# Kernel tuning notes

Measured on AMD Instinct MI355X. Metric: run time of the kernel, lower is better.

The kernel has to match this reference:

```python
import jax, jax.numpy as jnp
import numpy as np

SEQ_DIM = 256
PAIR_DIM = 128
N_HEADS = 8
HIDDEN = 32
B, L = 4, 512


def layer_norm(x, gamma, beta, eps=1e-5):
    mu = jnp.mean(x, axis=-1, keepdims=True)
    var = jnp.var(x, axis=-1, keepdims=True)
    return (x - mu) * jax.lax.rsqrt(var + eps) * gamma + beta


def setup_inputs() -> dict:
    key = jax.random.key(0)
    ks = jax.random.split(key, 12)
    d = N_HEADS * HIDDEN
    s = 0.02
    return {
        "seq": jax.random.normal(ks[0], (B, L, SEQ_DIM), jnp.float32),
        "pair": jax.random.normal(ks[1], (B, L, L, PAIR_DIM), jnp.float32),
        "ln_seq_g": jnp.ones((SEQ_DIM,), jnp.float32),
        "ln_seq_b": jnp.zeros((SEQ_DIM,), jnp.float32),
        "ln_pair_g": jnp.ones((PAIR_DIM,), jnp.float32),
        "ln_pair_b": jnp.zeros((PAIR_DIM,), jnp.float32),
        "W_b": jax.random.normal(ks[2], (PAIR_DIM, N_HEADS), jnp.float32) * s,
        "W_q": jax.random.normal(ks[3], (SEQ_DIM, d), jnp.float32) * s,
        "W_k": jax.random.normal(ks[4], (SEQ_DIM, d), jnp.float32) * s,
        "W_v": jax.random.normal(ks[5], (SEQ_DIM, d), jnp.float32) * s,
        "W_g": jax.random.normal(ks[6], (SEQ_DIM, d), jnp.float32) * s,
        "b_g": jnp.zeros((d,), jnp.float32),
        "W_o": jax.random.normal(ks[7], (d, SEQ_DIM), jnp.float32) * s,
        "b_o": jnp.zeros((SEQ_DIM,), jnp.float32),
    }


def reference(seq, pair, ln_seq_g, ln_seq_b, ln_pair_g, ln_pair_b,
              W_b, W_q, W_k, W_v, W_g, b_g, W_o, b_o):
    b, l, _ = seq.shape
    factor = 1.0 / np.sqrt(HIDDEN).astype(np.float32)
    s = layer_norm(seq, ln_seq_g, ln_seq_b)
    p = layer_norm(pair, ln_pair_g, ln_pair_b)
    Q = (s @ W_q).reshape(b, l, N_HEADS, HIDDEN)
    K = (s @ W_k).reshape(b, l, N_HEADS, HIDDEN)
    V = (s @ W_v).reshape(b, l, N_HEADS, HIDDEN)
    # pair bias: [b, i, j, n] -> [b, n, i, j]
    bias = jnp.einsum('bijp,pn->bnij', p, W_b)
    att = jnp.einsum('binh,bjnh->bnij', Q, K) * factor + bias
    att = jax.nn.softmax(att, axis=-1)
    gate = jax.nn.sigmoid(s @ W_g + b_g).reshape(b, l, N_HEADS, HIDDEN)
    out = jnp.einsum('bnij,bjnh->binh', att, V) * gate
    out = out.reshape(b, l, N_HEADS * HIDDEN)
    return out @ W_o + b_o
```

## Files before the change

kernel.cpp:

```cpp
#include <hip/hip_runtime.h>
#include <math.h>

#define OFF_Q    0
#define OFF_K    (524288)
#define OFF_V    (524288*2)
#define OFF_G    (524288*3)
#define OFF_PRE  (524288*4)
#define OFF_BIAS (524288*5)

template <int CTRL>
__device__ __forceinline__ float dpp_mov(float x) {
  return __int_as_float(__builtin_amdgcn_update_dpp(0, __float_as_int(x), CTRL, 0xF, 0xF, true));
}
template <int CTRL>
__device__ __forceinline__ float dpp_add(float x) { return x + dpp_mov<CTRL>(x); }
__device__ __forceinline__ float red16(float v) {
  v = dpp_add<0xB1>(v);
  v = dpp_add<0x4E>(v);
  v = dpp_add<0x141>(v);
  v = dpp_add<0x140>(v);
  return v;
}

#define SEL8(a, f, out) do { \
  float _s0 = ((f)&1) ? a[1] : a[0]; \
  float _s1 = ((f)&1) ? a[3] : a[2]; \
  float _s2 = ((f)&1) ? a[5] : a[4]; \
  float _s3 = ((f)&1) ? a[7] : a[6]; \
  float _t0 = ((f)&2) ? _s1 : _s0; \
  float _t1 = ((f)&2) ? _s3 : _s2; \
  out = ((f)&4) ? _t1 : _t0; \
} while(0)

__device__ __forceinline__ float4 sel8_f4(const float4* a, int f) {
  float4 s0 = (f&1) ? a[1] : a[0];
  float4 s1 = (f&1) ? a[3] : a[2];
  float4 s2 = (f&1) ? a[5] : a[4];
  float4 s3 = (f&1) ? a[7] : a[6];
  float4 t0 = (f&2) ? s1 : s0;
  float4 t1 = (f&2) ? s3 : s2;
  return (f&4) ? t1 : t0;
}

__device__ __forceinline__ float dot4(float4 a, float4 b, float acc) {
  acc = fmaf(a.x, b.x, acc); acc = fmaf(a.y, b.y, acc);
  acc = fmaf(a.z, b.z, acc); return fmaf(a.w, b.w, acc);
}

template <int CTRL>
__device__ __forceinline__ void merge_dpp(float& m, float& l, float4* acc) {
  float m2 = dpp_mov<CTRL>(m);
  float l2 = dpp_mov<CTRL>(l);
  float M = fmaxf(m, m2);
  float ea = __expf(m - M), eb = __expf(m2 - M);
  l = l*ea + l2*eb;
#pragma unroll
  for (int x = 0; x < 8; ++x) {
    acc[x].x = acc[x].x*ea + dpp_mov<CTRL>(acc[x].x)*eb;
    acc[x].y = acc[x].y*ea + dpp_mov<CTRL>(acc[x].y)*eb;
    acc[x].z = acc[x].z*ea + dpp_mov<CTRL>(acc[x].z)*eb;
    acc[x].w = acc[x].w*ea + dpp_mov<CTRL>(acc[x].w)*eb;
  }
  m = M;
}

__global__ __launch_bounds__(256, 3) void k_mega(
    const float* __restrict__ seq, const float* __restrict__ lsg, const float* __restrict__ lsb,
    const float* __restrict__ lpg, const float* __restrict__ lpb, const float* __restrict__ Wb,
    const float* __restrict__ Wq, const float* __restrict__ Wk, const float* __restrict__ Wv,
    const float* __restrict__ Wg, const float* __restrict__ bg, const float* __restrict__ pair,
    float* __restrict__ Qw, float* __restrict__ Kw, float* __restrict__ Vw, float* __restrict__ Gw,
    float* __restrict__ biasw) {
  __shared__ __align__(16) float As[256*36];
  int t = threadIdx.x;
  int blk = blockIdx.x;

  if (blk >= 512) {
    int kb = blk - 512;
    int m0 = (kb >> 3) * 32;
    int y = kb & 7;
    {
      int r = t >> 3, c0 = t & 7;
      const float* srow = seq + (size_t)(m0 + r) * 256;
      float4 v[8];
      float s = 0.f, sq = 0.f;
#pragma unroll
      for (int qq = 0; qq < 8; ++qq) {
        v[qq] = *(const float4*)(srow + 4*(c0 + 8*qq));
        s += v[qq].x + v[qq].y + v[qq].z + v[qq].w;
        sq = fmaf(v[qq].x, v[qq].x, sq); sq = fmaf(v[qq].y, v[qq].y, sq);
        sq = fmaf(v[qq].z, v[qq].z, sq); sq = fmaf(v[qq].w, v[qq].w, sq);
      }
#pragma unroll
      for (int mm = 1; mm < 8; mm <<= 1) { s += __shfl_xor(s, mm); sq += __shfl_xor(sq, mm); }
      float mu = s * (1.f/256.f);
      float var = sq * (1.f/256.f) - mu*mu;
      float rstd = rsqrtf(var + 1e-5f);
#pragma unroll
      for (int qq = 0; qq < 8; ++qq) {
        int c4 = c0 + 8*qq;
        float4 g  = *(const float4*)(lsg + 4*c4);
        float4 bb = *(const float4*)(lsb + 4*c4);
        float* dp = As + 4*c4*36 + r;
        dp[0]   = (v[qq].x - mu)*rstd*g.x + bb.x;
        dp[36]  = (v[qq].y - mu)*rstd*g.y + bb.y;
        dp[72]  = (v[qq].z - mu)*rstd*g.z + bb.z;
        dp[108] = (v[qq].w - mu)*rstd*g.w + bb.w;
      }
    }
    __syncthreads();
    const float* Wm = (y < 2) ? Wq : (y < 4) ? Wk : (y < 6) ? Wv : Wg;
    int cb = (y & 1) * 128;
    int rg = t >> 5, cg2 = t & 31;
    const float* bp = Wm + cb + 4*cg2;
    const float* ap = As + 4*rg;
    float4 a0 = {0,0,0,0}, a1 = {0,0,0,0}, a2 = {0,0,0,0}, a3 = {0,0,0,0};
#pragma unroll 4
    for (int p = 0; p < 256; ++p) {
      float4 a  = *(const float4*)(ap + p*36);
      float4 bv = *(const float4*)(bp + p*256);
      a0.x = fmaf(a.x, bv.x, a0.x); a0.y = fmaf(a.x, bv.y, a0.y);
      a0.z = fmaf(a.x, bv.z, a0.z); a0.w = fmaf(a.x, bv.w, a0.w);
      a1.x = fmaf(a.y, bv.x, a1.x); a1.y = fmaf(a.y, bv.y, a1.y);
      a1.z = fmaf(a.y, bv.z, a1.z); a1.w = fmaf(a.y, bv.w, a1.w);
      a2.x = fmaf(a.z, bv.x, a2.x); a2.y = fmaf(a.z, bv.y, a2.y);
      a2.z = fmaf(a.z, bv.z, a2.z); a2.w = fmaf(a.z, bv.w, a2.w);
      a3.x = fmaf(a.w, bv.x, a3.x); a3.y = fmaf(a.w, bv.y, a3.y);
      a3.z = fmaf(a.w, bv.z, a3.z); a3.w = fmaf(a.w, bv.w, a3.w);
    }
    int mat = y >> 1;
    int col = cb + 4*cg2;
    float* outp = (mat == 0) ? Qw : (mat == 1) ? Kw : (mat == 2) ? Vw : Gw;
    if (mat == 0) {
      const float qs = 0.17677669529663687f;
      a0.x*=qs; a0.y*=qs; a0.z*=qs; a0.w*=qs;
      a1.x*=qs; a1.y*=qs; a1.z*=qs; a1.w*=qs;
      a2.x*=qs; a2.y*=qs; a2.z*=qs; a2.w*=qs;
      a3.x*=qs; a3.y*=qs; a3.z*=qs; a3.w*=qs;
    }
    if (mat == 3) {
      float4 g4 = *(const float4*)(bg + col);
      a0.x = 1.f/(1.f+__expf(-(a0.x+g4.x))); a0.y = 1.f/(1.f+__expf(-(a0.y+g4.y)));
      a0.z = 1.f/(1.f+__expf(-(a0.z+g4.z))); a0.w = 1.f/(1.f+__expf(-(a0.w+g4.w)));
      a1.x = 1.f/(1.f+__expf(-(a1.x+g4.x))); a1.y = 1.f/(1.f+__expf(-(a1.y+g4.y)));
      a1.z = 1.f/(1.f+__expf(-(a1.z+g4.z))); a1.w = 1.f/(1.f+__expf(-(a1.w+g4.w)));
      a2.x = 1.f/(1.f+__expf(-(a2.x+g4.x))); a2.y = 1.f/(1.f+__expf(-(a2.y+g4.y)));
      a2.z = 1.f/(1.f+__expf(-(a2.z+g4.z))); a2.w = 1.f/(1.f+__expf(-(a2.w+g4.w)));
      a3.x = 1.f/(1.f+__expf(-(a3.x+g4.x))); a3.y = 1.f/(1.f+__expf(-(a3.y+g4.y)));
      a3.z = 1.f/(1.f+__expf(-(a3.z+g4.z))); a3.w = 1.f/(1.f+__expf(-(a3.w+g4.w)));
    }
    int orow = m0 + 4*rg;
    *(float4*)(outp + (size_t)(orow+0)*256 + col) = a0;
    *(float4*)(outp + (size_t)(orow+1)*256 + col) = a1;
    *(float4*)(outp + (size_t)(orow+2)*256 + col) = a2;
    *(float4*)(outp + (size_t)(orow+3)*256 + col) = a3;
    return;
  }

  int lane = t & 63, w = t >> 6;
  int grp = lane >> 4, f = lane & 15;

  float wp[64];
  float cg[8] = {0,0,0,0,0,0,0,0}, cbv[8] = {0,0,0,0,0,0,0,0};
#pragma unroll
  for (int q = 0; q < 4; ++q) {
    int kA = 4*f + q, kB = 64 + 4*f + q;
    float gA = lpg[kA], bA = lpb[kA];
    float gB = lpg[kB], bB = lpb[kB];
    float4 uA0 = *(const float4*)(Wb + kA*8);
    float4 uA1 = *(const float4*)(Wb + kA*8 + 4);
    float4 uB0 = *(const float4*)(Wb + kB*8);
    float4 uB1 = *(const float4*)(Wb + kB*8 + 4);
    wp[q*8+0] = gA*uA0.x; cg[0] += wp[q*8+0]; cbv[0] = fmaf(bA, uA0.x, cbv[0]);
    wp[q*8+1] = gA*uA0.y; cg[1] += wp[q*8+1]; cbv[1] = fmaf(bA, uA0.y, cbv[1]);
    wp[q*8+2] = gA*uA0.z; cg[2] += wp[q*8+2]; cbv[2] = fmaf(bA, uA0.z, cbv[2]);
    wp[q*8+3] = gA*uA0.w; cg[3] += wp[q*8+3]; cbv[3] = fmaf(bA, uA0.w, cbv[3]);
    wp[q*8+4] = gA*uA1.x; cg[4] += wp[q*8+4]; cbv[4] = fmaf(bA, uA1.x, cbv[4]);
    wp[q*8+5] = gA*uA1.y; cg[5] += wp[q*8+5]; cbv[5] = fmaf(bA, uA1.y, cbv[5]);
    wp[q*8+6] = gA*uA1.z; cg[6] += wp[q*8+6]; cbv[6] = fmaf(bA, uA1.z, cbv[6]);
    wp[q*8+7] = gA*uA1.w; cg[7] += wp[q*8+7]; cbv[7] = fmaf(bA, uA1.w, cbv[7]);
    int qb8 = (4+q)*8;
    wp[qb8+0] = gB*uB0.x; cg[0] += wp[qb8+0]; cbv[0] = fmaf(bB, uB0.x, cbv[0]);
    wp[qb8+1] = gB*uB0.y; cg[1] += wp[qb8+1]; cbv[1] = fmaf(bB, uB0.y, cbv[1]);
    wp[qb8+2] = gB*uB0.z; cg[2] += wp[qb8+2]; cbv[2] = fmaf(bB, uB0.z, cbv[2]);
    wp[qb8+3] = gB*uB0.w; cg[3] += wp[qb8+3]; cbv[3] = fmaf(bB, uB0.w, cbv[3]);
    wp[qb8+4] = gB*uB1.x; cg[4] += wp[qb8+4]; cbv[4] = fmaf(bB, uB1.x, cbv[4]);
    wp[qb8+5] = gB*uB1.y; cg[5] += wp[qb8+5]; cbv[5] = fmaf(bB, uB1.y, cbv[5]);
    wp[qb8+6] = gB*uB1.z; cg[6] += wp[qb8+6]; cbv[6] = fmaf(bB, uB1.z, cbv[6]);
    wp[qb8+7] = gB*uB1.w; cg[7] += wp[qb8+7]; cbv[7] = fmaf(bB, uB1.w, cbv[7]);
  }
#pragma unroll
  for (int n2 = 0; n2 < 8; ++n2) { cg[n2] = red16(cg[n2]); cbv[n2] = red16(cbv[n2]); }
  float cgsel, cbsel;
  SEL8(cg, f, cgsel);
  SEL8(cbv, f, cbsel);

  int gid = blk*16 + w*4 + grp;
  const float* rp0 = pair + (size_t)gid*128 + 4*f;
  float* bw0 = biasw + (size_t)gid*8 + f;

#define PROCROW(X0, X1, IDX) { \
    float s_  = X0.x + X0.y + X0.z + X0.w + X1.x + X1.y + X1.z + X1.w; \
    float sq_ = X0.x*X0.x; \
    sq_ = fmaf(X0.y, X0.y, sq_); sq_ = fmaf(X0.z, X0.z, sq_); sq_ = fmaf(X0.w, X0.w, sq_); \
    sq_ = fmaf(X1.x, X1.x, sq_); sq_ = fmaf(X1.y, X1.y, sq_); \
    sq_ = fmaf(X1.z, X1.z, sq_); sq_ = fmaf(X1.w, X1.w, sq_); \
    float dd_[8]; \
    _Pragma("unroll") \
    for (int n2 = 0; n2 < 8; ++n2) { \
      float d_ = X0.x * wp[n2]; \
      d_ = fmaf(X0.y, wp[8+n2],  d_); \
      d_ = fmaf(X0.z, wp[16+n2], d_); \
      d_ = fmaf(X0.w, wp[24+n2], d_); \
      d_ = fmaf(X1.x, wp[32+n2], d_); \
      d_ = fmaf(X1.y, wp[40+n2], d_); \
      d_ = fmaf(X1.z, wp[48+n2], d_); \
      d_ = fmaf(X1.w, wp[56+n2], d_); \
      dd_[n2] = d_; \
    } \
    s_  = red16(s_); \
    sq_ = red16(sq_); \
    _Pragma("unroll") \
    for (int n2 = 0; n2 < 8; ++n2) dd_[n2] = red16(dd_[n2]); \
    float mu_ = s_ * (1.f/128.f); \
    float var_ = fmaf(sq_, 1.f/128.f, -mu_*mu_); \
    float rstd_ = rsqrtf(var_ + 1e-5f); \
    if (f < 8) { \
      float dv_; \
      SEL8(dd_, f, dv_); \
      bw0[(size_t)(IDX)*65536] = fmaf(rstd_, fmaf(-mu_, cgsel, dv_), cbsel); \
    } \
  }

  float4 A0[4], A1[4], B0[4], B1[4];
#pragma unroll
  for (int q = 0; q < 4; ++q) {
    const float* r = rp0 + (size_t)q*1048576;
    A0[q] = *(const float4*)r; A1[q] = *(const float4*)(r + 64);
  }
#pragma unroll
  for (int q = 0; q < 4; ++q) {
    const float* r = rp0 + (size_t)(4+q)*1048576;
    B0[q] = *(const float4*)r; B1[q] = *(const float4*)(r + 64);
  }

#define CHUNK(C0, C1, cc) { \
    _Pragma("unroll") \
    for (int q = 0; q < 4; ++q) PROCROW(C0[q], C1[q], (4*(cc) + q)); \
    if ((cc) + 2 < 32) { \
      _Pragma("unroll") \
      for (int q = 0; q < 4; ++q) { \
        const float* r = rp0 + (size_t)(4*((cc)+2) + q)*1048576; \
        C0[q] = *(const float4*)r; C1[q] = *(const float4*)(r + 64); \
      } \
    } \
  }

  for (int c = 0; c < 32; c += 2) {
    CHUNK(A0, A1, c)
    CHUNK(B0, B1, c+1)
  }
#undef CHUNK
#undef PROCROW
}

__global__ __launch_bounds__(256, 2) void k_attn6(
    const float* __restrict__ Qw, const float* __restrict__ Kw, const float* __restrict__ Vw,
    const float* __restrict__ Gw, const float* __restrict__ biasw, float* __restrict__ prew) {
  __shared__ __align__(16) float Kb[2][16*292];
  __shared__ __align__(16) float Vb[2][16*292];
  float* scr = &Kb[0][0];

  int t = threadIdx.x, lane = t & 63, w = t >> 6;
  int b = blockIdx.x >> 7;
  int i0 = (blockIdx.x & 127) << 2;
  int n = lane >> 3, js = lane & 7;
  int ip = w & 1, jset = w >> 1;
  int ila = 2*ip, ilb = ila + 1;
  size_t qra = (size_t)(b*512 + i0 + ila);
  size_t qrb = qra + 1;
  int jl0 = jset*8 + js;

  float4 qa[8], qb[8];
  {
    const float* pa = Qw + qra*256 + n*32;
    const float* pb = Qw + qrb*256 + n*32;
#pragma unroll
    for (int x = 0; x < 8; ++x) { qa[x] = *(const float4*)(pa + 4*x); qb[x] = *(const float4*)(pb + 4*x); }
  }
  float4 acca[8], accb[8];
#pragma unroll
  for (int x = 0; x < 8; ++x) { acca[x] = make_float4(0,0,0,0); accb[x] = make_float4(0,0,0,0); }
  float ma = -1e30f, la = 0.f, mb2 = -1e30f, lb2 = 0.f;

  const float* Kg = Kw + (size_t)(b*512)*256;
  const float* Vg = Vw + (size_t)(b*512)*256;
  const float* Bpa = biasw + ((size_t)(b*512 + i0 + ila)*512 + jl0)*8 + n;
  const float* Bpb = Bpa + 512*8;

  float4 sk[4], sv[4];
  int woff = (lane >> 3)*36 + (lane & 7)*4;

#define SLOAD(tn) { \
    const float* ks_ = Kg + ((size_t)(tn)*16 + 4*w)*256 + 4*lane; \
    const float* vs_ = Vg + ((size_t)(tn)*16 + 4*w)*256 + 4*lane; \
    sk[0] = *(const float4*)(ks_);       sk[1] = *(const float4*)(ks_ + 256); \
    sk[2] = *(const float4*)(ks_ + 512); sk[3] = *(const float4*)(ks_ + 768); \
    sv[0] = *(const float4*)(vs_);       sv[1] = *(const float4*)(vs_ + 256); \
    sv[2] = *(const float4*)(vs_ + 512); sv[3] = *(const float4*)(vs_ + 768); \
  }
#define SWRITE(tn) { int bf_ = (tn) & 1; \
    float* kd_ = &Kb[bf_][(4*w)*292 + woff]; \
    *(float4*)(kd_)       = sk[0]; *(float4*)(kd_ + 292) = sk[1]; \
    *(float4*)(kd_ + 584) = sk[2]; *(float4*)(kd_ + 876) = sk[3]; \
    float* vd_ = &Vb[bf_][(4*w)*292 + woff]; \
    *(float4*)(vd_)       = sv[0]; *(float4*)(vd_ + 292) = sv[1]; \
    *(float4*)(vd_ + 584) = sv[2]; *(float4*)(vd_ + 876) = sv[3]; \
  }

  SLOAD(0);
  SWRITE(0);
  __syncthreads();

  for (int tt = 0; tt < 32; ++tt) {
    int cur = tt & 1;
    if (tt < 31) SLOAD(tt+1);

    const float* Kt = Kb[cur];
    const float* Vt = Vb[cur];
    float bba = Bpa[tt*128];
    float bbb = Bpb[tt*128];

    float lga, lgb;
    {
      const float* kp = Kt + jl0*292 + n*36;
      float da = 0.f, db = 0.f;
#pragma unroll
      for (int x = 0; x < 8; ++x) {
        float4 kk = *(const float4*)(kp + 4*x);
        da = dot4(qa[x], kk, da); db = dot4(qb[x], kk, db);
      }
      lga = da + bba; lgb = db + bbb;
    }
    if (lga > ma) {
      float sc = __expf(ma - lga);
      la *= sc;
#pragma unroll
      for (int x = 0; x < 8; ++x) {
        acca[x].x *= sc; acca[x].y *= sc; acca[x].z *= sc; acca[x].w *= sc;
      }
      ma = lga;
    }
    if (lgb > mb2) {
      float sc = __expf(mb2 - lgb);
      lb2 *= sc;
#pragma unroll
      for (int x = 0; x < 8; ++x) {
        accb[x].x *= sc; accb[x].y *= sc; accb[x].z *= sc; accb[x].w *= sc;
      }
      mb2 = lgb;
    }
    float pa_ = __expf(lga - ma), pb_ = __expf(lgb - mb2);
    la += pa_; lb2 += pb_;
    {
      const float* vp = Vt + jl0*292 + n*36;
#pragma unroll
      for (int x = 0; x < 8; ++x) {
        float4 vv = *(const float4*)(vp + 4*x);
        acca[x].x = fmaf(pa_, vv.x, acca[x].x); acca[x].y = fmaf(pa_, vv.y, acca[x].y);
        acca[x].z = fmaf(pa_, vv.z, acca[x].z); acca[x].w = fmaf(pa_, vv.w, acca[x].w);
        accb[x].x = fmaf(pb_, vv.x, accb[x].x); accb[x].y = fmaf(pb_, vv.y, accb[x].y);
        accb[x].z = fmaf(pb_, vv.z, accb[x].z); accb[x].w = fmaf(pb_, vv.w, accb[x].w);
      }
    }

    if (tt < 31) SWRITE(tt+1);
    __syncthreads();
  }
#undef SLOAD
#undef SWRITE

  merge_dpp<0xB1>(ma, la, acca);   merge_dpp<0xB1>(mb2, lb2, accb);
  merge_dpp<0x4E>(ma, la, acca);   merge_dpp<0x4E>(mb2, lb2, accb);
  merge_dpp<0x141>(ma, la, acca);  merge_dpp<0x141>(mb2, lb2, accb);

  float4 fa = sel8_f4(acca, js);
  float4 fb = sel8_f4(accb, js);

  if (jset == 1) {
    int base = (ip*8 + n)*68;
    *(float4*)(scr + base + 4*js) = fa;
    *(float4*)(scr + base + 32 + 4*js) = fb;
    if (js == 0) { scr[base+64] = ma; scr[base+65] = la; scr[base+66] = mb2; scr[base+67] = lb2; }
  }
  __syncthreads();
  if (jset == 0) {
    int base = (ip*8 + n)*68;
    float4 a2 = *(const float4*)(scr + base + 4*js);
    float4 b2 = *(const float4*)(scr + base + 32 + 4*js);
    float m2a = scr[base+64], l2a = scr[base+65];
    float m2b = scr[base+66], l2b = scr[base+67];
    {
      float M = fmaxf(ma, m2a);
      float ea = __expf(ma - M), eb = __expf(m2a - M);
      float inv = 1.f / (la*ea + l2a*eb);
      float4 g4 = *(const float4*)(Gw + qra*256 + n*32 + 4*js);
      float4 r;
      r.x = (fa.x*ea + a2.x*eb) * inv * g4.x;
      r.y = (fa.y*ea + a2.y*eb) * inv * g4.y;
      r.z = (fa.z*ea + a2.z*eb) * inv * g4.z;
      r.w = (fa.w*ea + a2.w*eb) * inv * g4.w;
      *(float4*)(prew + qra*256 + n*32 + 4*js) = r;
    }
    {
      float M = fmaxf(mb2, m2b);
      float ea = __expf(mb2 - M), eb = __expf(m2b - M);
      float inv = 1.f / (lb2*ea + l2b*eb);
      float4 g4 = *(const float4*)(Gw + qrb*256 + n*32 + 4*js);
      float4 r;
      r.x = (fb.x*ea + b2.x*eb) * inv * g4.x;
      r.y = (fb.y*ea + b2.y*eb) * inv * g4.y;
      r.z = (fb.z*ea + b2.z*eb) * inv * g4.z;
      r.w = (fb.w*ea + b2.w*eb) * inv * g4.w;
      *(float4*)(prew + qrb*256 + n*32 + 4*js) = r;
    }
  }
}

__global__ __launch_bounds__(256) void k_out(
    const float* __restrict__ prew, const float* __restrict__ Wo, const float* __restrict__ bo,
    float* __restrict__ out) {
  __shared__ __align__(16) float As[256*36];
  int t = threadIdx.x;
  int m0 = blockIdx.x * 32;
  int y = blockIdx.y;
  {
    int r = t >> 3, c0 = t & 7;
    const float* srow = prew + (size_t)(m0 + r)*256;
#pragma unroll
    for (int qq = 0; qq < 8; ++qq) {
      int c4 = c0 + 8*qq;
      float4 v = *(const float4*)(srow + 4*c4);
      float* dp = As + 4*c4*36 + r;
      dp[0] = v.x; dp[36] = v.y; dp[72] = v.z; dp[108] = v.w;
    }
  }
  __syncthreads();
  int cb = y*128;
  int rg = t >> 5, cg2 = t & 31;
  int col = cb + 4*cg2;
  const float* bp = Wo + col;
  const float* ap = As + 4*rg;
  float4 a0 = {0,0,0,0}, a1 = {0,0,0,0}, a2 = {0,0,0,0}, a3 = {0,0,0,0};
#pragma unroll 4
  for (int p = 0; p < 256; ++p) {
    float4 a  = *(const float4*)(ap + p*36);
    float4 bv = *(const float4*)(bp + p*256);
    a0.x = fmaf(a.x, bv.x, a0.x); a0.y = fmaf(a.x, bv.y, a0.y);
    a0.z = fmaf(a.x, bv.z, a0.z); a0.w = fmaf(a.x, bv.w, a0.w);
    a1.x = fmaf(a.y, bv.x, a1.x); a1.y = fmaf(a.y, bv.y, a1.y);
    a1.z = fmaf(a.y, bv.z, a1.z); a1.w = fmaf(a.y, bv.w, a1.w);
    a2.x = fmaf(a.z, bv.x, a2.x); a2.y = fmaf(a.z, bv.y, a2.y);
    a2.z = fmaf(a.z, bv.z, a2.z); a2.w = fmaf(a.z, bv.w, a2.w);
    a3.x = fmaf(a.w, bv.x, a3.x); a3.y = fmaf(a.w, bv.y, a3.y);
    a3.z = fmaf(a.w, bv.z, a3.z); a3.w = fmaf(a.w, bv.w, a3.w);
  }
  float4 b4 = *(const float4*)(bo + col);
  a0.x += b4.x; a0.y += b4.y; a0.z += b4.z; a0.w += b4.w;
  a1.x += b4.x; a1.y += b4.y; a1.z += b4.z; a1.w += b4.w;
  a2.x += b4.x; a2.y += b4.y; a2.z += b4.z; a2.w += b4.w;
  a3.x += b4.x; a3.y += b4.y; a3.z += b4.z; a3.w += b4.w;
  int orow = m0 + 4*rg;
  *(float4*)(out + (size_t)(orow+0)*256 + col) = a0;
  *(float4*)(out + (size_t)(orow+1)*256 + col) = a1;
  *(float4*)(out + (size_t)(orow+2)*256 + col) = a2;
  *(float4*)(out + (size_t)(orow+3)*256 + col) = a3;
}

extern "C" void kernel_launch(void* const* d_in, const int* in_sizes, int n_in,
                              void* d_out, int out_size, void* d_ws, size_t ws_size,
                              hipStream_t stream) {
  const float* seq  = (const float*)d_in[0];
  const float* pair = (const float*)d_in[1];
  const float* lsg  = (const float*)d_in[2];
  const float* lsb  = (const float*)d_in[3];
  const float* lpg  = (const float*)d_in[4];
  const float* lpb  = (const float*)d_in[5];
  const float* Wb   = (const float*)d_in[6];
  const float* Wq   = (const float*)d_in[7];
  const float* Wk   = (const float*)d_in[8];
  const float* Wv   = (const float*)d_in[9];
  const float* Wg   = (const float*)d_in[10];
  const float* bg   = (const float*)d_in[11];
  const float* Wo   = (const float*)d_in[12];
  const float* bo   = (const float*)d_in[13];
  float* ws   = (float*)d_ws;
  float* Qw   = ws + OFF_Q;
  float* Kw   = ws + OFF_K;
  float* Vw   = ws + OFF_V;
  float* Gw   = ws + OFF_G;
  float* prew = ws + OFF_PRE;
  float* biasw= ws + OFF_BIAS;
  float* out  = (float*)d_out;

  hipLaunchKernelGGL(k_mega, dim3(1024), dim3(256), 0, stream,
                     seq, lsg, lsb, lpg, lpb, Wb, Wq, Wk, Wv, Wg, bg, pair,
                     Qw, Kw, Vw, Gw, biasw);
  hipLaunchKernelGGL(k_attn6, dim3(512), dim3(256), 0, stream,
                     Qw, Kw, Vw, Gw, biasw, prew);
  hipLaunchKernelGGL(k_out, dim3(64, 2), dim3(256), 0, stream,
                     prew, Wo, bo, out);
}
```

Before: 214.8 us.

## Fuse pair-bias layernorm projection into attention kernel with producer warps

The pair layernorm plus bias projection moves out of the first mega-kernel and into the attention kernel. Four of eight warps per 512-thread block now produce bias tiles from the pair tensor into a double-buffered shared memory buffer, while the other four run the online-softmax attention over 32-key tiles. This removes the global write and re-read of the bias tensor (B*L*L*8 floats). In exchange, the pair read now happens inside the attention kernel instead of overlapping with the QKVG projection, and shared memory per block grows.

```diff
diff --git a/kernel.cpp b/kernel.cpp
--- a/kernel.cpp
+++ b/kernel.cpp
@@ -6,7 +6,6 @@
 #define OFF_V    (524288*2)
 #define OFF_G    (524288*3)
 #define OFF_PRE  (524288*4)
-#define OFF_BIAS (524288*5)
 
 template <int CTRL>
 __device__ __forceinline__ float dpp_mov(float x) {
@@ -64,142 +63,255 @@
   m = M;
 }
 
-__global__ __launch_bounds__(256, 3) void k_mega(
+__global__ __launch_bounds__(256, 3) void k_qkvg(
     const float* __restrict__ seq, const float* __restrict__ lsg, const float* __restrict__ lsb,
-    const float* __restrict__ lpg, const float* __restrict__ lpb, const float* __restrict__ Wb,
     const float* __restrict__ Wq, const float* __restrict__ Wk, const float* __restrict__ Wv,
-    const float* __restrict__ Wg, const float* __restrict__ bg, const float* __restrict__ pair,
-    float* __restrict__ Qw, float* __restrict__ Kw, float* __restrict__ Vw, float* __restrict__ Gw,
-    float* __restrict__ biasw) {
+    const float* __restrict__ Wg, const float* __restrict__ bg,
+    float* __restrict__ Qw, float* __restrict__ Kw, float* __restrict__ Vw, float* __restrict__ Gw) {
   __shared__ __align__(16) float As[256*36];
   int t = threadIdx.x;
   int blk = blockIdx.x;
-
-  if (blk >= 512) {
-    int kb = blk - 512;
-    int m0 = (kb >> 3) * 32;
-    int y = kb & 7;
+  int m0 = (blk >> 3) * 32;
+  int y = blk & 7;
+  {
+    int r = t >> 3, c0 = t & 7;
+    const float* srow = seq + (size_t)(m0 + r) * 256;
+    float4 v[8];
+    float s = 0.f, sq = 0.f;
+#pragma unroll
+    for (int qq = 0; qq < 8; ++qq) {
+      v[qq] = *(const float4*)(srow + 4*(c0 + 8*qq));
+      s += v[qq].x + v[qq].y + v[qq].z + v[qq].w;
+      sq = fmaf(v[qq].x, v[qq].x, sq); sq = fmaf(v[qq].y, v[qq].y, sq);
+      sq = fmaf(v[qq].z, v[qq].z, sq); sq = fmaf(v[qq].w, v[qq].w, sq);
+    }
+#pragma unroll
+    for (int mm = 1; mm < 8; mm <<= 1) { s += __shfl_xor(s, mm); sq += __shfl_xor(sq, mm); }
+    float mu = s * (1.f/256.f);
+    float var = sq * (1.f/256.f) - mu*mu;
+    float rstd = rsqrtf(var + 1e-5f);
+#pragma unroll
+    for (int qq = 0; qq < 8; ++qq) {
+      int c4 = c0 + 8*qq;
+      float4 g  = *(const float4*)(lsg + 4*c4);
+      float4 bb = *(const float4*)(lsb + 4*c4);
+      float* dp = As + 4*c4*36 + r;
+      dp[0]   = (v[qq].x - mu)*rstd*g.x + bb.x;
+      dp[36]  = (v[qq].y - mu)*rstd*g.y + bb.y;
+      dp[72]  = (v[qq].z - mu)*rstd*g.z + bb.z;
+      dp[108] = (v[qq].w - mu)*rstd*g.w + bb.w;
+    }
+  }
+  __syncthreads();
+  const float* Wm = (y < 2) ? Wq : (y < 4) ? Wk : (y < 6) ? Wv : Wg;
+  int cb = (y & 1) * 128;
+  int rg = t >> 5, cg2 = t & 31;
+  const float* bp = Wm + cb + 4*cg2;
+  const float* ap = As + 4*rg;
+  float4 a0 = {0,0,0,0}, a1 = {0,0,0,0}, a2 = {0,0,0,0}, a3 = {0,0,0,0};
+#pragma unroll 4
+  for (int p = 0; p < 256; ++p) {
+    float4 a  = *(const float4*)(ap + p*36);
+    float4 bv = *(const float4*)(bp + p*256);
+    a0.x = fmaf(a.x, bv.x, a0.x); a0.y = fmaf(a.x, bv.y, a0.y);
+    a0.z = fmaf(a.x, bv.z, a0.z); a0.w = fmaf(a.x, bv.w, a0.w);
+    a1.x = fmaf(a.y, bv.x, a1.x); a1.y = fmaf(a.y, bv.y, a1.y);
+    a1.z = fmaf(a.y, bv.z, a1.z); a1.w = fmaf(a.y, bv.w, a1.w);
+    a2.x = fmaf(a.z, bv.x, a2.x); a2.y = fmaf(a.z, bv.y, a2.y);
+    a2.z = fmaf(a.z, bv.z, a2.z); a2.w = fmaf(a.z, bv.w, a2.w);
+    a3.x = fmaf(a.w, bv.x, a3.x); a3.y = fmaf(a.w, bv.y, a3.y);
+    a3.z = fmaf(a.w, bv.z, a3.z); a3.w = fmaf(a.w, bv.w, a3.w);
+  }
+  int mat = y >> 1;
+  int col = cb + 4*cg2;
+  float* outp = (mat == 0) ? Qw : (mat == 1) ? Kw : (mat == 2) ? Vw : Gw;
+  if (mat == 0) {
+    const float qs = 0.17677669529663687f;
+    a0.x*=qs; a0.y*=qs; a0.z*=qs; a0.w*=qs;
+    a1.x*=qs; a1.y*=qs; a1.z*=qs; a1.w*=qs;
+    a2.x*=qs; a2.y*=qs; a2.z*=qs; a2.w*=qs;
+    a3.x*=qs; a3.y*=qs; a3.z*=qs; a3.w*=qs;
+  }
+  if (mat == 3) {
+    float4 g4 = *(const float4*)(bg + col);
+    a0.x = 1.f/(1.f+__expf(-(a0.x+g4.x))); a0.y = 1.f/(1.f+__expf(-(a0.y+g4.y)));
+    a0.z = 1.f/(1.f+__expf(-(a0.z+g4.z))); a0.w = 1.f/(1.f+__expf(-(a0.w+g4.w)));
+    a1.x = 1.f/(1.f+__expf(-(a1.x+g4.x))); a1.y = 1.f/(1.f+__expf(-(a1.y+g4.y)));
+    a1.z = 1.f/(1.f+__expf(-(a1.z+g4.z))); a1.w = 1.f/(1.f+__expf(-(a1.w+g4.w)));
+    a2.x = 1.f/(1.f+__expf(-(a2.x+g4.x))); a2.y = 1.f/(1.f+__expf(-(a2.y+g4.y)));
+    a2.z = 1.f/(1.f+__expf(-(a2.z+g4.z))); a2.w = 1.f/(1.f+__expf(-(a2.w+g4.w)));
+    a3.x = 1.f/(1.f+__expf(-(a3.x+g4.x))); a3.y = 1.f/(1.f+__expf(-(a3.y+g4.y)));
+    a3.z = 1.f/(1.f+__expf(-(a3.z+g4.z))); a3.w = 1.f/(1.f+__expf(-(a3.w+g4.w)));
+  }
+  int orow = m0 + 4*rg;
+  *(float4*)(outp + (size_t)(orow+0)*256 + col) = a0;
+  *(float4*)(outp + (size_t)(orow+1)*256 + col) = a1;
+  *(float4*)(outp + (size_t)(orow+2)*256 + col) = a2;
+  *(float4*)(outp + (size_t)(orow+3)*256 + col) = a3;
+}
+
+#define KVS 292
+__global__ __launch_bounds__(512, 2) void k_fused(
+    const float* __restrict__ Qw, const float* __restrict__ Kw, const float* __restrict__ Vw,
+    const float* __restrict__ Gw, const float* __restrict__ lpg, const float* __restrict__ lpb,
+    const float* __restrict__ Wb, const float* __restrict__ pair, float* __restrict__ prew) {
+  __shared__ __align__(16) float Kb[2][32*KVS];
+  __shared__ __align__(16) float Vb[2][32*KVS];
+  __shared__ __align__(16) float Bbuf[2][1024];
+  float* scr = &Kb[0][0];
+
+  int t = threadIdx.x, lane = t & 63, w = t >> 6;
+  int b = blockIdx.x >> 7, i0 = (blockIdx.x & 127) << 2;
+
+  const float* Kg = Kw + (size_t)(b*512)*256;
+  const float* Vg = Vw + (size_t)(b*512)*256;
+  float4 sk[4], sv[4];
+  int woff = (lane >> 3)*36 + (lane & 7)*4;
+
+  int n = lane >> 3, js = lane & 7;
+  int ip = w & 1, jset = (w >> 1) & 1;
+  int ila = 2*ip, ilb = ila + 1;
+  size_t qra = (size_t)(b*512 + i0 + ila);
+  size_t qrb = qra + 1;
+  float4 fa, fb;
+  float ma = -1e30f, la = 0.f, mb2 = -1e30f, lb2 = 0.f;
+
+#define SLOAD(tn) { \
+    const float* ks_ = Kg + ((size_t)(tn)*32 + 4*w)*256 + 4*lane; \
+    const float* vs_ = Vg + ((size_t)(tn)*32 + 4*w)*256 + 4*lane; \
+    sk[0] = *(const float4*)(ks_);       sk[1] = *(const float4*)(ks_ + 256); \
+    sk[2] = *(const float4*)(ks_ + 512); sk[3] = *(const float4*)(ks_ + 768); \
+    sv[0] = *(const float4*)(vs_);       sv[1] = *(const float4*)(vs_ + 256); \
+    sv[2] = *(const float4*)(vs_ + 512); sv[3] = *(const float4*)(vs_ + 768); \
+  }
+#define SWRITE(tn) { int bf_ = (tn) & 1; \
+    float* kd_ = &Kb[bf_][(4*w)*KVS + woff]; \
+    *(float4*)(kd_)         = sk[0]; *(float4*)(kd_ + KVS)   = sk[1]; \
+    *(float4*)(kd_ + 2*KVS) = sk[2]; *(float4*)(kd_ + 3*KVS) = sk[3]; \
+    float* vd_ = &Vb[bf_][(4*w)*KVS + woff]; \
+    *(float4*)(vd_)         = sv[0]; *(float4*)(vd_ + KVS)   = sv[1]; \
+    *(float4*)(vd_ + 2*KVS) = sv[2]; *(float4*)(vd_ + 3*KVS) = sv[3]; \
+  }
+
+  if (w < 4) {
+    float4 qa[8], qb[8];
     {
-      int r = t >> 3, c0 = t & 7;
-      const float* srow = seq + (size_t)(m0 + r) * 256;
-      float4 v[8];
-      float s = 0.f, sq = 0.f;
-#pragma unroll
-      for (int qq = 0; qq < 8; ++qq) {
-        v[qq] = *(const float4*)(srow + 4*(c0 + 8*qq));
-        s += v[qq].x + v[qq].y + v[qq].z + v[qq].w;
-        sq = fmaf(v[qq].x, v[qq].x, sq); sq = fmaf(v[qq].y, v[qq].y, sq);
-        sq = fmaf(v[qq].z, v[qq].z, sq); sq = fmaf(v[qq].w, v[qq].w, sq);
+      const float* pa = Qw + qra*256 + n*32;
+      const float* pb = Qw + qrb*256 + n*32;
+#pragma unroll
+      for (int x = 0; x < 8; ++x) { qa[x] = *(const float4*)(pa + 4*x); qb[x] = *(const float4*)(pb + 4*x); }
+    }
+    float4 acca[8], accb[8];
+#pragma unroll
+    for (int x = 0; x < 8; ++x) { acca[x] = make_float4(0,0,0,0); accb[x] = make_float4(0,0,0,0); }
+
+    SLOAD(0);
+    SWRITE(0);
+    __syncthreads();
+
+    for (int tt = 0; tt < 16; ++tt) {
+      int cur = tt & 1;
+      if (tt < 15) SLOAD(tt+1);
+      const float* Kt = Kb[cur];
+      const float* Vt = Vb[cur];
+      const float* Bt = Bbuf[cur];
+#pragma unroll
+      for (int jj2 = 0; jj2 < 2; ++jj2) {
+        int jl = jset*16 + jj2*8 + js;
+        float bba = Bt[(ila*32 + jl)*8 + n];
+        float bbb = Bt[(ilb*32 + jl)*8 + n];
+        const float* kp = Kt + jl*KVS + n*36;
+        float da = 0.f, db = 0.f;
+#pragma unroll
+        for (int x = 0; x < 8; ++x) {
+          float4 kk = *(const float4*)(kp + 4*x);
+          da = dot4(qa[x], kk, da); db = dot4(qb[x], kk, db);
+        }
+        float lga = da + bba, lgb = db + bbb;
+        if (lga > ma) {
+          float sc = __expf(ma - lga);
+          la *= sc;
+#pragma unroll
+          for (int x = 0; x < 8; ++x) {
+            acca[x].x *= sc; acca[x].y *= sc; acca[x].z *= sc; acca[x].w *= sc;
+          }
+          ma = lga;
+        }
+        if (lgb > mb2) {
+          float sc = __expf(mb2 - lgb);
+          lb2 *= sc;
+#pragma unroll
+          for (int x = 0; x < 8; ++x) {
+            accb[x].x *= sc; accb[x].y *= sc; accb[x].z *= sc; accb[x].w *= sc;
+          }
+          mb2 = lgb;
+        }
+        float pa_ = __expf(lga - ma), pb_ = __expf(lgb - mb2);
+        la += pa_; lb2 += pb_;
+        const float* vp = Vt + jl*KVS + n*36;
+#pragma unroll
+        for (int x = 0; x < 8; ++x) {
+          float4 vv = *(const float4*)(vp + 4*x);
+          acca[x].x = fmaf(pa_, vv.x, acca[x].x); acca[x].y = fmaf(pa_, vv.y, acca[x].y);
+          acca[x].z = fmaf(pa_, vv.z, acca[x].z); acca[x].w = fmaf(pa_, vv.w, acca[x].w);
+          accb[x].x = fmaf(pb_, vv.x, accb[x].x); accb[x].y = fmaf(pb_, vv.y, accb[x].y);
+          accb[x].z = fmaf(pb_, vv.z, accb[x].z); accb[x].w = fmaf(pb_, vv.w, accb[x].w);
+        }
       }
-#pragma unroll
-      for (int mm = 1; mm < 8; mm <<= 1) { s += __shfl_xor(s, mm); sq += __shfl_xor(sq, mm); }
-      float mu = s * (1.f/256.f);
-      float var = sq * (1.f/256.f) - mu*mu;
-      float rstd = rsqrtf(var + 1e-5f);
-#pragma unroll
-      for (int qq = 0; qq < 8; ++qq) {
-        int c4 = c0 + 8*qq;
-        float4 g  = *(const float4*)(lsg + 4*c4);
-        float4 bb = *(const float4*)(lsb + 4*c4);
-        float* dp = As + 4*c4*36 + r;
-        dp[0]   = (v[qq].x - mu)*rstd*g.x + bb.x;
-        dp[36]  = (v[qq].y - mu)*rstd*g.y + bb.y;
-        dp[72]  = (v[qq].z - mu)*rstd*g.z + bb.z;
-        dp[108] = (v[qq].w - mu)*rstd*g.w + bb.w;
-      }
-    }
-    __syncthreads();
-    const float* Wm = (y < 2) ? Wq : (y < 4) ? Wk : (y < 6) ? Wv : Wg;
-    int cb = (y & 1) * 128;
-    int rg = t >> 5, cg2 = t & 31;
-    const float* bp = Wm + cb + 4*cg2;
-    const float* ap = As + 4*rg;
-    float4 a0 = {0,0,0,0}, a1 = {0,0,0,0}, a2 = {0,0,0,0}, a3 = {0,0,0,0};
-#pragma unroll 4
-    for (int p = 0; p < 256; ++p) {
-      float4 a  = *(const float4*)(ap + p*36);
-      float4 bv = *(const float4*)(bp + p*256);
-      a0.x = fmaf(a.x, bv.x, a0.x); a0.y = fmaf(a.x, bv.y, a0.y);
-      a0.z = fmaf(a.x, bv.z, a0.z); a0.w = fmaf(a.x, bv.w, a0.w);
-      a1.x = fmaf(a.y, bv.x, a1.x); a1.y = fmaf(a.y, bv.y, a1.y);
-      a1.z = fmaf(a.y, bv.z, a1.z); a1.w = fmaf(a.y, bv.w, a1.w);
-      a2.x = fmaf(a.z, bv.x, a2.x); a2.y = fmaf(a.z, bv.y, a2.y);
-      a2.z = fmaf(a.z, bv.z, a2.z); a2.w = fmaf(a.z, bv.w, a2.w);
-      a3.x = fmaf(a.w, bv.x, a3.x); a3.y = fmaf(a.w, bv.y, a3.y);
-      a3.z = fmaf(a.w, bv.z, a3.z); a3.w = fmaf(a.w, bv.w, a3.w);
-    }
-    int mat = y >> 1;
-    int col = cb + 4*cg2;
-    float* outp = (mat == 0) ? Qw : (mat == 1) ? Kw : (mat == 2) ? Vw : Gw;
-    if (mat == 0) {
-      const float qs = 0.17677669529663687f;
-      a0.x*=qs; a0.y*=qs; a0.z*=qs; a0.w*=qs;
-      a1.x*=qs; a1.y*=qs; a1.z*=qs; a1.w*=qs;
-      a2.x*=qs; a2.y*=qs; a2.z*=qs; a2.w*=qs;
-      a3.x*=qs; a3.y*=qs; a3.z*=qs; a3.w*=qs;
-    }
-    if (mat == 3) {
-      float4 g4 = *(const float4*)(bg + col);
-      a0.x = 1.f/(1.f+__expf(-(a0.x+g4.x))); a0.y = 1.f/(1.f+__expf(-(a0.y+g4.y)));
-      a0.z = 1.f/(1.f+__expf(-(a0.z+g4.z))); a0.w = 1.f/(1.f+__expf(-(a0.w+g4.w)));
-      a1.x = 1.f/(1.f+__expf(-(a1.x+g4.x))); a1.y = 1.f/(1.f+__expf(-(a1.y+g4.y)));
-      a1.z = 1.f/(1.f+__expf(-(a1.z+g4.z))); a1.w = 1.f/(1.f+__expf(-(a1.w+g4.w)));
-      a2.x = 1.f/(1.f+__expf(-(a2.x+g4.x))); a2.y = 1.f/(1.f+__expf(-(a2.y+g4.y)));
-      a2.z = 1.f/(1.f+__expf(-(a2.z+g4.z))); a2.w = 1.f/(1.f+__expf(-(a2.w+g4.w)));
-      a3.x = 1.f/(1.f+__expf(-(a3.x+g4.x))); a3.y = 1.f/(1.f+__expf(-(a3.y+g4.y)));
-      a3.z = 1.f/(1.f+__expf(-(a3.z+g4.z))); a3.w = 1.f/(1.f+__expf(-(a3.w+g4.w)));
-    }
-    int orow = m0 + 4*rg;
-    *(float4*)(outp + (size_t)(orow+0)*256 + col) = a0;
-    *(float4*)(outp + (size_t)(orow+1)*256 + col) = a1;
-    *(float4*)(outp + (size_t)(orow+2)*256 + col) = a2;
-    *(float4*)(outp + (size_t)(orow+3)*256 + col) = a3;
-    return;
-  }
-
-  int lane = t & 63, w = t >> 6;
-  int grp = lane >> 4, f = lane & 15;
-
-  float wp[64];
-  float cg[8] = {0,0,0,0,0,0,0,0}, cbv[8] = {0,0,0,0,0,0,0,0};
-#pragma unroll
-  for (int q = 0; q < 4; ++q) {
-    int kA = 4*f + q, kB = 64 + 4*f + q;
-    float gA = lpg[kA], bA = lpb[kA];
-    float gB = lpg[kB], bB = lpb[kB];
-    float4 uA0 = *(const float4*)(Wb + kA*8);
-    float4 uA1 = *(const float4*)(Wb + kA*8 + 4);
-    float4 uB0 = *(const float4*)(Wb + kB*8);
-    float4 uB1 = *(const float4*)(Wb + kB*8 + 4);
-    wp[q*8+0] = gA*uA0.x; cg[0] += wp[q*8+0]; cbv[0] = fmaf(bA, uA0.x, cbv[0]);
-    wp[q*8+1] = gA*uA0.y; cg[1] += wp[q*8+1]; cbv[1] = fmaf(bA, uA0.y, cbv[1]);
-    wp[q*8+2] = gA*uA0.z; cg[2] += wp[q*8+2]; cbv[2] = fmaf(bA, uA0.z, cbv[2]);
-    wp[q*8+3] = gA*uA0.w; cg[3] += wp[q*8+3]; cbv[3] = fmaf(bA, uA0.w, cbv[3]);
-    wp[q*8+4] = gA*uA1.x; cg[4] += wp[q*8+4]; cbv[4] = fmaf(bA, uA1.x, cbv[4]);
-    wp[q*8+5] = gA*uA1.y; cg[5] += wp[q*8+5]; cbv[5] = fmaf(bA, uA1.y, cbv[5]);
-    wp[q*8+6] = gA*uA1.z; cg[6] += wp[q*8+6]; cbv[6] = fmaf(bA, uA1.z, cbv[6]);
-    wp[q*8+7] = gA*uA1.w; cg[7] += wp[q*8+7]; cbv[7] = fmaf(bA, uA1.w, cbv[7]);
-    int qb8 = (4+q)*8;
-    wp[qb8+0] = gB*uB0.x; cg[0] += wp[qb8+0]; cbv[0] = fmaf(bB, uB0.x, cbv[0]);
-    wp[qb8+1] = gB*uB0.y; cg[1] += wp[qb8+1]; cbv[1] = fmaf(bB, uB0.y, cbv[1]);
-    wp[qb8+2] = gB*uB0.z; cg[2] += wp[qb8+2]; cbv[2] = fmaf(bB, uB0.z, cbv[2]);
-    wp[qb8+3] = gB*uB0.w; cg[3] += wp[qb8+3]; cbv[3] = fmaf(bB, uB0.w, cbv[3]);
-    wp[qb8+4] = gB*uB1.x; cg[4] += wp[qb8+4]; cbv[4] = fmaf(bB, uB1.x, cbv[4]);
-    wp[qb8+5] = gB*uB1.y; cg[5] += wp[qb8+5]; cbv[5] = fmaf(bB, uB1.y, cbv[5]);
-    wp[qb8+6] = gB*uB1.z; cg[6] += wp[qb8+6]; cbv[6] = fmaf(bB, uB1.z, cbv[6]);
-    wp[qb8+7] = gB*uB1.w; cg[7] += wp[qb8+7]; cbv[7] = fmaf(bB, uB1.w, cbv[7]);
-  }
-#pragma unroll
-  for (int n2 = 0; n2 < 8; ++n2) { cg[n2] = red16(cg[n2]); cbv[n2] = red16(cbv[n2]); }
-  float cgsel, cbsel;
-  SEL8(cg, f, cgsel);
-  SEL8(cbv, f, cbsel);
-
-  int gid = blk*16 + w*4 + grp;
-  const float* rp0 = pair + (size_t)gid*128 + 4*f;
-  float* bw0 = biasw + (size_t)gid*8 + f;
-
-#define PROCROW(X0, X1, IDX) { \
+      if (tt < 15) SWRITE(tt+1);
+      __syncthreads();
+    }
+
+    merge_dpp<0xB1>(ma, la, acca);   merge_dpp<0xB1>(mb2, lb2, accb);
+    merge_dpp<0x4E>(ma, la, acca);   merge_dpp<0x4E>(mb2, lb2, accb);
+    merge_dpp<0x141>(ma, la, acca);  merge_dpp<0x141>(mb2, lb2, accb);
+    fa = sel8_f4(acca, js);
+    fb = sel8_f4(accb, js);
+  } else {
+    int w4 = w - 4;
+    int grp = lane >> 4, f = lane & 15;
+    int g = w4*4 + grp;
+    int il = g >> 2;
+    int jjbase = (g & 3) * 8;
+
+    float wp[64];
+    float cg[8] = {0,0,0,0,0,0,0,0}, cbv[8] = {0,0,0,0,0,0,0,0};
+#pragma unroll
+    for (int q = 0; q < 4; ++q) {
+      int kA = 4*f + q, kB = 64 + 4*f + q;
+      float gA = lpg[kA], bA = lpb[kA];
+      float gB = lpg[kB], bB = lpb[kB];
+      float4 uA0 = *(const float4*)(Wb + kA*8);
+      float4 uA1 = *(const float4*)(Wb + kA*8 + 4);
+      float4 uB0 = *(const float4*)(Wb + kB*8);
+      float4 uB1 = *(const float4*)(Wb + kB*8 + 4);
+      wp[q*8+0] = gA*uA0.x; cg[0] += wp[q*8+0]; cbv[0] = fmaf(bA, uA0.x, cbv[0]);
+      wp[q*8+1] = gA*uA0.y; cg[1] += wp[q*8+1]; cbv[1] = fmaf(bA, uA0.y, cbv[1]);
+      wp[q*8+2] = gA*uA0.z; cg[2] += wp[q*8+2]; cbv[2] = fmaf(bA, uA0.z, cbv[2]);
+      wp[q*8+3] = gA*uA0.w; cg[3] += wp[q*8+3]; cbv[3] = fmaf(bA, uA0.w, cbv[3]);
+      wp[q*8+4] = gA*uA1.x; cg[4] += wp[q*8+4]; cbv[4] = fmaf(bA, uA1.x, cbv[4]);
+      wp[q*8+5] = gA*uA1.y; cg[5] += wp[q*8+5]; cbv[5] = fmaf(bA, uA1.y, cbv[5]);
+      wp[q*8+6] = gA*uA1.z; cg[6] += wp[q*8+6]; cbv[6] = fmaf(bA, uA1.z, cbv[6]);
+      wp[q*8+7] = gA*uA1.w; cg[7] += wp[q*8+7]; cbv[7] = fmaf(bA, uA1.w, cbv[7]);
+      int qb8 = (4+q)*8;
+      wp[qb8+0] = gB*uB0.x; cg[0] += wp[qb8+0]; cbv[0] = fmaf(bB, uB0.x, cbv[0]);
+      wp[qb8+1] = gB*uB0.y; cg[1] += wp[qb8+1]; cbv[1] = fmaf(bB, uB0.y, cbv[1]);
+      wp[qb8+2] = gB*uB0.z; cg[2] += wp[qb8+2]; cbv[2] = fmaf(bB, uB0.z, cbv[2]);
+      wp[qb8+3] = gB*uB0.w; cg[3] += wp[qb8+3]; cbv[3] = fmaf(bB, uB0.w, cbv[3]);
+      wp[qb8+4] = gB*uB1.x; cg[4] += wp[qb8+4]; cbv[4] = fmaf(bB, uB1.x, cbv[4]);
+      wp[qb8+5] = gB*uB1.y; cg[5] += wp[qb8+5]; cbv[5] = fmaf(bB, uB1.y, cbv[5]);
+      wp[qb8+6] = gB*uB1.z; cg[6] += wp[qb8+6]; cbv[6] = fmaf(bB, uB1.z, cbv[6]);
+      wp[qb8+7] = gB*uB1.w; cg[7] += wp[qb8+7]; cbv[7] = fmaf(bB, uB1.w, cbv[7]);
+    }
+#pragma unroll
+    for (int n2 = 0; n2 < 8; ++n2) { cg[n2] = red16(cg[n2]); cbv[n2] = red16(cbv[n2]); }
+    float cgsel, cbsel;
+    SEL8(cg, f, cgsel);
+    SEL8(cbv, f, cbsel);
+
+    size_t prowbase = (size_t)(b*512 + i0 + il) * 512;
+
+#define PROCB(X0, X1, JJ, PB) { \
     float s_  = X0.x + X0.y + X0.z + X0.w + X1.x + X1.y + X1.z + X1.w; \
     float sq_ = X0.x*X0.x; \
     sq_ = fmaf(X0.y, X0.y, sq_); sq_ = fmaf(X0.z, X0.z, sq_); sq_ = fmaf(X0.w, X0.w, sq_); \
@@ -228,173 +340,57 @@
     if (f < 8) { \
       float dv_; \
       SEL8(dd_, f, dv_); \
-      bw0[(size_t)(IDX)*65536] = fmaf(rstd_, fmaf(-mu_, cgsel, dv_), cbsel); \
+      Bbuf[PB][(il*32 + (JJ))*8 + f] = fmaf(rstd_, fmaf(-mu_, cgsel, dv_), cbsel); \
     } \
   }
 
-  float4 A0[4], A1[4], B0[4], B1[4];
-#pragma unroll
-  for (int q = 0; q < 4; ++q) {
-    const float* r = rp0 + (size_t)q*1048576;
-    A0[q] = *(const float4*)r; A1[q] = *(const float4*)(r + 64);
-  }
-#pragma unroll
-  for (int q = 0; q < 4; ++q) {
-    const float* r = rp0 + (size_t)(4+q)*1048576;
-    B0[q] = *(const float4*)r; B1[q] = *(const float4*)(r + 64);
-  }
-
-#define CHUNK(C0, C1, cc) { \
+#define LOADB(D0, D1, SB, J0G) { \
     _Pragma("unroll") \
-    for (int q = 0; q < 4; ++q) PROCROW(C0[q], C1[q], (4*(cc) + q)); \
-    if ((cc) + 2 < 32) { \
-      _Pragma("unroll") \
-      for (int q = 0; q < 4; ++q) { \
-        const float* r = rp0 + (size_t)(4*((cc)+2) + q)*1048576; \
-        C0[q] = *(const float4*)r; C1[q] = *(const float4*)(r + 64); \
-      } \
-    } \
-  }
-
-  for (int c = 0; c < 32; c += 2) {
-    CHUNK(A0, A1, c)
-    CHUNK(B0, B1, c+1)
-  }
-#undef CHUNK
-#undef PROCROW
-}
-
-__global__ __launch_bounds__(256, 2) void k_attn6(
-    const float* __restrict__ Qw, const float* __restrict__ Kw, const float* __restrict__ Vw,
-    const float* __restrict__ Gw, const float* __restrict__ biasw, float* __restrict__ prew) {
-  __shared__ __align__(16) float Kb[2][16*292];
-  __shared__ __align__(16) float Vb[2][16*292];
-  float* scr = &Kb[0][0];
-
-  int t = threadIdx.x, lane = t & 63, w = t >> 6;
-  int b = blockIdx.x >> 7;
-  int i0 = (blockIdx.x & 127) << 2;
-  int n = lane >> 3, js = lane & 7;
-  int ip = w & 1, jset = w >> 1;
-  int ila = 2*ip, ilb = ila + 1;
-  size_t qra = (size_t)(b*512 + i0 + ila);
-  size_t qrb = qra + 1;
-  int jl0 = jset*8 + js;
-
-  float4 qa[8], qb[8];
-  {
-    const float* pa = Qw + qra*256 + n*32;
-    const float* pb = Qw + qrb*256 + n*32;
-#pragma unroll
-    for (int x = 0; x < 8; ++x) { qa[x] = *(const float4*)(pa + 4*x); qb[x] = *(const float4*)(pb + 4*x); }
-  }
-  float4 acca[8], accb[8];
-#pragma unroll
-  for (int x = 0; x < 8; ++x) { acca[x] = make_float4(0,0,0,0); accb[x] = make_float4(0,0,0,0); }
-  float ma = -1e30f, la = 0.f, mb2 = -1e30f, lb2 = 0.f;
-
-  const float* Kg = Kw + (size_t)(b*512)*256;
-  const float* Vg = Vw + (size_t)(b*512)*256;
-  const float* Bpa = biasw + ((size_t)(b*512 + i0 + ila)*512 + jl0)*8 + n;
-  const float* Bpb = Bpa + 512*8;
-
-  float4 sk[4], sv[4];
-  int woff = (lane >> 3)*36 + (lane & 7)*4;
-
-#define SLOAD(tn) { \
-    const float* ks_ = Kg + ((size_t)(tn)*16 + 4*w)*256 + 4*lane; \
-    const float* vs_ = Vg + ((size_t)(tn)*16 + 4*w)*256 + 4*lane; \
-    sk[0] = *(const float4*)(ks_);       sk[1] = *(const float4*)(ks_ + 256); \
-    sk[2] = *(const float4*)(ks_ + 512); sk[3] = *(const float4*)(ks_ + 768); \
-    sv[0] = *(const float4*)(vs_);       sv[1] = *(const float4*)(vs_ + 256); \
-    sv[2] = *(const float4*)(vs_ + 512); sv[3] = *(const float4*)(vs_ + 768); \
-  }
-#define SWRITE(tn) { int bf_ = (tn) & 1; \
-    float* kd_ = &Kb[bf_][(4*w)*292 + woff]; \
-    *(float4*)(kd_)       = sk[0]; *(float4*)(kd_ + 292) = sk[1]; \
-    *(float4*)(kd_ + 584) = sk[2]; *(float4*)(kd_ + 876) = sk[3]; \
-    float* vd_ = &Vb[bf_][(4*w)*292 + woff]; \
-    *(float4*)(vd_)       = sv[0]; *(float4*)(vd_ + 292) = sv[1]; \
-    *(float4*)(vd_ + 584) = sv[2]; *(float4*)(vd_ + 876) = sv[3]; \
-  }
-
-  SLOAD(0);
-  SWRITE(0);
-  __syncthreads();
-
-  for (int tt = 0; tt < 32; ++tt) {
-    int cur = tt & 1;
-    if (tt < 31) SLOAD(tt+1);
-
-    const float* Kt = Kb[cur];
-    const float* Vt = Vb[cur];
-    float bba = Bpa[tt*128];
-    float bbb = Bpb[tt*128];
-
-    float lga, lgb;
-    {
-      const float* kp = Kt + jl0*292 + n*36;
-      float da = 0.f, db = 0.f;
-#pragma unroll
-      for (int x = 0; x < 8; ++x) {
-        float4 kk = *(const float4*)(kp + 4*x);
-        da = dot4(qa[x], kk, da); db = dot4(qb[x], kk, db);
+    for (int q2 = 0; q2 < 4; ++q2) { \
+      const float* r_ = pair + (prowbase + (size_t)(J0G) + (size_t)(jjbase + (SB)*4 + q2))*128 + 4*f; \
+      D0[q2] = *(const float4*)r_; D1[q2] = *(const float4*)(r_ + 64); \
+    } }
+#define PROCB4(S0, S1, SB, PB) { \
+    _Pragma("unroll") \
+    for (int q2 = 0; q2 < 4; ++q2) { PROCB(S0[q2], S1[q2], (jjbase + (SB)*4 + q2), PB) } }
+
+#define PRODUCE(PB, J0G) { \
+    float4 XA0[4], XA1[4], XB0[4], XB1[4]; \
+    LOADB(XA0, XA1, 0, J0G) \
+    LOADB(XB0, XB1, 1, J0G) \
+    PROCB4(XA0, XA1, 0, PB) \
+    PROCB4(XB0, XB1, 1, PB) \
+  }
+
+    SLOAD(0);
+    PRODUCE(0, 0)
+    SWRITE(0);
+    __syncthreads();
+
+    for (int tt = 0; tt < 16; ++tt) {
+      if (tt < 15) {
+        SLOAD(tt+1);
+        PRODUCE((tt+1) & 1, (tt+1)*32)
+        SWRITE(tt+1);
       }
-      lga = da + bba; lgb = db + bbb;
-    }
-    if (lga > ma) {
-      float sc = __expf(ma - lga);
-      la *= sc;
-#pragma unroll
-      for (int x = 0; x < 8; ++x) {
-        acca[x].x *= sc; acca[x].y *= sc; acca[x].z *= sc; acca[x].w *= sc;
-      }
-      ma = lga;
-    }
-    if (lgb > mb2) {
-      float sc = __expf(mb2 - lgb);
-      lb2 *= sc;
-#pragma unroll
-      for (int x = 0; x < 8; ++x) {
-        accb[x].x *= sc; accb[x].y *= sc; accb[x].z *= sc; accb[x].w *= sc;
-      }
-      mb2 = lgb;
-    }
-    float pa_ = __expf(lga - ma), pb_ = __expf(lgb - mb2);
-    la += pa_; lb2 += pb_;
-    {
-      const float* vp = Vt + jl0*292 + n*36;
-#pragma unroll
-      for (int x = 0; x < 8; ++x) {
-        float4 vv = *(const float4*)(vp + 4*x);
-        acca[x].x = fmaf(pa_, vv.x, acca[x].x); acca[x].y = fmaf(pa_, vv.y, acca[x].y);
-        acca[x].z = fmaf(pa_, vv.z, acca[x].z); acca[x].w = fmaf(pa_, vv.w, acca[x].w);
-        accb[x].x = fmaf(pb_, vv.x, accb[x].x); accb[x].y = fmaf(pb_, vv.y, accb[x].y);
-        accb[x].z = fmaf(pb_, vv.z, accb[x].z); accb[x].w = fmaf(pb_, vv.w, accb[x].w);
-      }
-    }
-
-    if (tt < 31) SWRITE(tt+1);
-    __syncthreads();
+      __syncthreads();
+    }
+#undef PRODUCE
+#undef PROCB4
+#undef LOADB
+#undef PROCB
   }
 #undef SLOAD
 #undef SWRITE
 
-  merge_dpp<0xB1>(ma, la, acca);   merge_dpp<0xB1>(mb2, lb2, accb);
-  merge_dpp<0x4E>(ma, la, acca);   merge_dpp<0x4E>(mb2, lb2, accb);
-  merge_dpp<0x141>(ma, la, acca);  merge_dpp<0x141>(mb2, lb2, accb);
-
-  float4 fa = sel8_f4(acca, js);
-  float4 fb = sel8_f4(accb, js);
-
-  if (jset == 1) {
+  if (w < 4 && jset == 1) {
     int base = (ip*8 + n)*68;
     *(float4*)(scr + base + 4*js) = fa;
     *(float4*)(scr + base + 32 + 4*js) = fb;
     if (js == 0) { scr[base+64] = ma; scr[base+65] = la; scr[base+66] = mb2; scr[base+67] = lb2; }
   }
   __syncthreads();
-  if (jset == 0) {
+  if (w < 4 && jset == 0) {
     int base = (ip*8 + n)*68;
     float4 a2 = *(const float4*)(scr + base + 4*js);
     float4 b2 = *(const float4*)(scr + base + 32 + 4*js);
@@ -500,14 +496,12 @@
   float* Vw   = ws + OFF_V;
   float* Gw   = ws + OFF_G;
   float* prew = ws + OFF_PRE;
-  float* biasw= ws + OFF_BIAS;
   float* out  = (float*)d_out;
 
-  hipLaunchKernelGGL(k_mega, dim3(1024), dim3(256), 0, stream,
-                     seq, lsg, lsb, lpg, lpb, Wb, Wq, Wk, Wv, Wg, bg, pair,
-                     Qw, Kw, Vw, Gw, biasw);
-  hipLaunchKernelGGL(k_attn6, dim3(512), dim3(256), 0, stream,
-                     Qw, Kw, Vw, Gw, biasw, prew);
+  hipLaunchKernelGGL(k_qkvg, dim3(512), dim3(256), 0, stream,
+                     seq, lsg, lsb, Wq, Wk, Wv, Wg, bg, Qw, Kw, Vw, Gw);
+  hipLaunchKernelGGL(k_fused, dim3(512), dim3(512), 0, stream,
+                     Qw, Kw, Vw, Gw, lpg, lpb, Wb, pair, prew);
   hipLaunchKernelGGL(k_out, dim3(64, 2), dim3(256), 0, stream,
                      prew, Wo, bo, out);
 }
```

Result: slower. 224.9 us (+4.7%).
